# Optimization experiments

Measured on AMD Instinct MI355X. Metric: run time of the kernel, lower is better.

## Reference

```python
import jax, jax.numpy as jnp
import numpy as np


def _log_g(x):
    # log of g(x) = x + 0.5 for x >= 0, sigmoid(x) for x < 0 (minGRU paper, log-space)
    return jnp.where(x >= 0, jnp.log(jax.nn.relu(x) + 0.5), -jax.nn.softplus(-x))


def setup_inputs() -> dict:
    key = jax.random.key(0)
    k1, k2, k3 = jax.random.split(key, 3)
    B, L, D, H = 4, 8192, 512, 1024
    x = jax.random.normal(k1, (B, L, D), dtype=jnp.float32)
    # 1x1 conv in-projection to [hidden | gate], scaled for sane activation magnitudes
    W_in = jax.random.normal(k2, (2 * H, D), dtype=jnp.float32) * 0.05
    b_in = jnp.zeros((2 * H,), dtype=jnp.float32)
    # 1x1 conv out-projection back to model dim
    W_out = jax.random.normal(k3, (D, H), dtype=jnp.float32) * 0.05
    b_out = jnp.zeros((D,), dtype=jnp.float32)
    return {"x": x, "W_in": W_in, "b_in": b_in, "W_out": W_out, "b_out": b_out}


def reference(x, W_in, b_in, W_out, b_out):
    # x: [B, L, D]. tokenMixer transposes to [B, D, L] for MinGRU (1x1 convs),
    # which is equivalent to pointwise matmuls over the channel dim here.
    hg = jnp.einsum('bld,ed->ble', x, W_in) + b_in          # [B, L, 2H]
    H = hg.shape[-1] // 2
    hidden, gate = hg[..., :H], hg[..., H:]

    # minGRU log-space parallel scan (Heinsen associative scan):
    # h_t = (1 - z_t) * h_{t-1} + z_t * g(hidden_t), z_t = sigmoid(gate_t)
    log_coeffs = -jax.nn.softplus(gate)      # log(1 - z_t)
    log_z = -jax.nn.softplus(-gate)          # log(z_t)
    log_tilde_h = _log_g(hidden)             # log(g(hidden_t))

    a_star = jnp.cumsum(log_coeffs, axis=1)                              # [B, L, H]
    log_h = a_star + jax.lax.cumlogsumexp(log_z + log_tilde_h - a_star, axis=1)
    h = jnp.exp(log_h)                                                   # [B, L, H]

    out = jnp.einsum('blh,dh->bld', h, W_out) + b_out                    # [B, L, D]
    return out
```

## Files before the change

kernel.cpp:

```cpp
#include <hip/hip_runtime.h>
#include <hip/hip_bf16.h>
#include <cstdint>
#include <cstddef>

#define B_ 4
#define L_ 8192
#define D_ 512
#define H_ 1024
#define NC_ 256
#define LC_ (L_ / NC_)

typedef float  f32x4 __attribute__((ext_vector_type(4)));
typedef short  s16x8 __attribute__((ext_vector_type(8)));
typedef __bf16 b16x8 __attribute__((ext_vector_type(8)));

template <typename T, typename U>
__device__ inline auto mfma_sel(T a, T b, f32x4 c, U, int)
    -> decltype(__builtin_amdgcn_mfma_f32_16x16x32_bf16(a, b, c, 0, 0, 0)) {
  return __builtin_amdgcn_mfma_f32_16x16x32_bf16(a, b, c, 0, 0, 0);
}
template <typename T, typename U>
__device__ inline f32x4 mfma_sel(T a, T b, f32x4 c, U, long) {
  return __builtin_amdgcn_mfma_f32_16x16x32_bf16(
      __builtin_bit_cast(U, a), __builtin_bit_cast(U, b), c, 0, 0, 0);
}
__device__ inline f32x4 mfma_bf16_16x16x32(s16x8 a, s16x8 b, f32x4 c) {
  return mfma_sel(a, b, c, b16x8{}, 0);
}

__device__ inline ushort f2bf(float f) {
  uint32_t u = __builtin_bit_cast(uint32_t, f);
  uint32_t r = (u + 0x7fffu + ((u >> 16) & 1u)) >> 16;
  return (ushort)r;
}
__device__ inline float bf2f(ushort u) {
  return __builtin_bit_cast(float, (uint32_t)u << 16);
}

__global__ void cast_kernel(const float* __restrict__ in, ushort* __restrict__ out, int n4) {
  int i = blockIdx.x * blockDim.x + threadIdx.x;
  if (i >= n4) return;
  float4 f = reinterpret_cast<const float4*>(in)[i];
  ushort4 o;
  o.x = f2bf(f.x); o.y = f2bf(f.y); o.z = f2bf(f.z); o.w = f2bf(f.w);
  reinterpret_cast<ushort4*>(out)[i] = o;
}

__global__ void cast2_kernel(const float* __restrict__ in0, ushort* __restrict__ out0, int n4_0,
                             const float* __restrict__ in1, ushort* __restrict__ out1, int n4_1) {
  int i = blockIdx.x * blockDim.x + threadIdx.x;
  const float* in; ushort* out;
  if (i < n4_0) { in = in0; out = out0; }
  else { i -= n4_0; if (i >= n4_1) return; in = in1; out = out1; }
  float4 f = reinterpret_cast<const float4*>(in)[i];
  ushort4 o;
  o.x = f2bf(f.x); o.y = f2bf(f.y); o.z = f2bf(f.z); o.w = f2bf(f.w);
  reinterpret_cast<ushort4*>(out)[i] = o;
}

#define GLDS(srcp, dstp)                                                            \
  __builtin_amdgcn_global_load_lds(                                                 \
      (const __attribute__((address_space(1))) void*)(srcp),                        \
      (__attribute__((address_space(3))) void*)(dstp), 16, 0, 0)

#define BAR()                               \
  do {                                      \
    asm volatile("" ::: "memory");          \
    __builtin_amdgcn_s_barrier();           \
    asm volatile("" ::: "memory");          \
  } while (0)

template <bool OUT_BF16>
__global__ __launch_bounds__(512, 2)
void gemm_bt(const ushort* __restrict__ A, const ushort* __restrict__ Bm,
             const float* __restrict__ bias, void* __restrict__ Cv,
             int M, int N, int K) {
  __shared__ ushort As[2][256 * 64];
  __shared__ ushort Bs[2][256 * 64];
  const int tid  = threadIdx.x;
  const int wave = tid >> 6;
  const int lane = tid & 63;
  const int l15  = lane & 15;
  const int quad = lane >> 4;

  int id = blockIdx.y * gridDim.x + blockIdx.x;
  const int nwg = gridDim.x * gridDim.y;
  id = (id & 7) * (nwg >> 3) + (id >> 3);
  const int bxi = id % gridDim.x;
  const int byi = id / gridDim.x;

  const long bm = (long)byi * 256;
  const long bn = (long)bxi * 256;
  const int  wm = (wave >> 2) * 128;
  const int  wn = (wave & 3) * 64;

  f32x4 acc[8][4];
#pragma unroll
  for (int i = 0; i < 8; ++i)
#pragma unroll
    for (int j = 0; j < 4; ++j) acc[i][j] = (f32x4){0.f, 0.f, 0.f, 0.f};

  const int rl  = lane >> 3;
  const int cb  = (lane & 7) ^ rl;
  const int srow = wave * 32 + rl;
  const ushort* gA0 = A  + (bm + srow) * (long)K + cb * 8;
  const ushort* gB0 = Bm + (bn + srow) * (long)K + cb * 8;
  int ldst[4];
#pragma unroll
  for (int i = 0; i < 4; ++i) ldst[i] = (wave * 32 + 8 * i) * 64;

  const int sq0 = ((0 * 4 + quad) ^ (l15 & 7)) * 8;
  const int sq1 = ((1 * 4 + quad) ^ (l15 & 7)) * 8;
  int arow[8], brow[4];
#pragma unroll
  for (int i = 0; i < 8; ++i) arow[i] = (wm + i * 16 + l15) * 64;
#pragma unroll
  for (int j = 0; j < 4; ++j) brow[j] = (wn + j * 16 + l15) * 64;

  const int nkt = K >> 6;

#pragma unroll
  for (int i = 0; i < 4; ++i) GLDS(gA0 + 8L * i * K, &As[0][ldst[i]]);
#pragma unroll
  for (int i = 0; i < 4; ++i) GLDS(gB0 + 8L * i * K, &Bs[0][ldst[i]]);
  asm volatile("s_waitcnt vmcnt(0)" ::: "memory");
  BAR();

  for (int t = 0; t < nkt; ++t) {
    const int buf  = t & 1;
    const int nbuf = buf ^ 1;
    const bool pf  = (t + 1) < nkt;
    const ushort* Ac = As[buf];
    const ushort* Bc = Bs[buf];
    const long koff = (long)(t + 1) * 64;
    s16x8 bf[4], af[4];

#pragma unroll
    for (int j = 0; j < 4; ++j)
      bf[j] = *reinterpret_cast<const s16x8*>(&Bc[brow[j] + sq0]);
#pragma unroll
    for (int i = 0; i < 4; ++i)
      af[i] = *reinterpret_cast<const s16x8*>(&Ac[arow[i] + sq0]);
    if (pf) {
#pragma unroll
      for (int i = 0; i < 4; ++i) GLDS(gA0 + 8L * i * K + koff, &As[nbuf][ldst[i]]);
    }
    BAR();
    __builtin_amdgcn_s_setprio(1);
#pragma unroll
    for (int i = 0; i < 4; ++i)
#pragma unroll
      for (int j = 0; j < 4; ++j)
        acc[i][j] = mfma_bf16_16x16x32(af[i], bf[j], acc[i][j]);
    __builtin_amdgcn_s_setprio(0);
    BAR();

#pragma unroll
    for (int i = 0; i < 4; ++i)
      af[i] = *reinterpret_cast<const s16x8*>(&Ac[arow[4 + i] + sq0]);
    if (pf) {
#pragma unroll
      for (int i = 0; i < 4; ++i) GLDS(gB0 + 8L * i * K + koff, &Bs[nbuf][ldst[i]]);
    }
    BAR();
    __builtin_amdgcn_s_setprio(1);
#pragma unroll
    for (int i = 0; i < 4; ++i)
#pragma unroll
      for (int j = 0; j < 4; ++j)
        acc[4 + i][j] = mfma_bf16_16x16x32(af[i], bf[j], acc[4 + i][j]);
    __builtin_amdgcn_s_setprio(0);
    BAR();

#pragma unroll
    for (int j = 0; j < 4; ++j)
      bf[j] = *reinterpret_cast<const s16x8*>(&Bc[brow[j] + sq1]);
#pragma unroll
    for (int i = 0; i < 4; ++i)
      af[i] = *reinterpret_cast<const s16x8*>(&Ac[arow[i] + sq1]);
    BAR();
    __builtin_amdgcn_s_setprio(1);
#pragma unroll
    for (int i = 0; i < 4; ++i)
#pragma unroll
      for (int j = 0; j < 4; ++j)
        acc[i][j] = mfma_bf16_16x16x32(af[i], bf[j], acc[i][j]);
    __builtin_amdgcn_s_setprio(0);
    BAR();

#pragma unroll
    for (int i = 0; i < 4; ++i)
      af[i] = *reinterpret_cast<const s16x8*>(&Ac[arow[4 + i] + sq1]);
    BAR();
    __builtin_amdgcn_s_setprio(1);
#pragma unroll
    for (int i = 0; i < 4; ++i)
#pragma unroll
      for (int j = 0; j < 4; ++j)
        acc[4 + i][j] = mfma_bf16_16x16x32(af[i], bf[j], acc[4 + i][j]);
    __builtin_amdgcn_s_setprio(0);
    if (pf) asm volatile("s_waitcnt vmcnt(0)" ::: "memory");
    BAR();
  }

#pragma unroll
  for (int mi = 0; mi < 8; ++mi) {
    const long mrow = bm + wm + mi * 16 + quad * 4;
#pragma unroll
    for (int ni = 0; ni < 4; ++ni) {
      const long ncol = bn + wn + ni * 16 + l15;
      const float bv = bias[ncol];
      if (OUT_BF16) {
        ushort* cp = (ushort*)Cv + mrow * (long)N + ncol;
#pragma unroll
        for (int r = 0; r < 4; ++r) cp[(long)r * N] = f2bf(acc[mi][ni][r] + bv);
      } else {
        float* cp = (float*)Cv + mrow * (long)N + ncol;
#pragma unroll
        for (int r = 0; r < 4; ++r) cp[(long)r * N] = acc[mi][ni][r] + bv;
      }
    }
  }
}

__device__ inline float softplus_f(float x) {
  return fmaxf(x, 0.f) + __logf(1.f + __expf(-fabsf(x)));
}
__device__ inline float logaddexp_f(float a, float b) {
  float m = fmaxf(a, b);
  return m + __logf(1.f + __expf(-fabsf(a - b)));
}
__device__ inline void transform_f(float hd, float g, float& lc, float& v) {
  float sp = softplus_f(g);
  lc = -sp;
  float lz = g - sp;
  float lth = (hd >= 0.f) ? __logf(hd + 0.5f) : (hd - softplus_f(hd));
  v = lz + lth;
}

__global__ void scan_phase1(const ushort* __restrict__ hg,
                            float* __restrict__ Ac, float* __restrict__ Bc) {
  int gid = blockIdx.x * blockDim.x + threadIdx.x;
  int hq = gid & (H_ / 4 - 1);
  int c  = (gid >> 8) & (NC_ - 1);
  int b  = gid >> 16;
  const ushort* p = hg + ((size_t)(b * L_ + c * LC_) * (2 * H_)) + hq * 4;
  float As[4] = {0.f, 0.f, 0.f, 0.f};
  float Bv[4] = {-INFINITY, -INFINITY, -INFINITY, -INFINITY};
#pragma unroll 4
  for (int l = 0; l < LC_; ++l) {
    ushort4 hd4 = *reinterpret_cast<const ushort4*>(p);
    ushort4 g4  = *reinterpret_cast<const ushort4*>(p + H_);
    float hdv[4] = {bf2f(hd4.x), bf2f(hd4.y), bf2f(hd4.z), bf2f(hd4.w)};
    float gv[4]  = {bf2f(g4.x),  bf2f(g4.y),  bf2f(g4.z),  bf2f(g4.w)};
#pragma unroll
    for (int j = 0; j < 4; ++j) {
      float lc, v; transform_f(hdv[j], gv[j], lc, v);
      As[j] += lc;
      Bv[j] = logaddexp_f(Bv[j] + lc, v);
    }
    p += 2 * H_;
  }
  size_t o = (size_t)(b * NC_ + c) * H_ + hq * 4;
  *reinterpret_cast<float4*>(&Ac[o]) = make_float4(As[0], As[1], As[2], As[3]);
  *reinterpret_cast<float4*>(&Bc[o]) = make_float4(Bv[0], Bv[1], Bv[2], Bv[3]);
}

__global__ void scan_phase2(const float* __restrict__ Ac, const float* __restrict__ Bc,
                            float* __restrict__ carry) {
  int gid = blockIdx.x * blockDim.x + threadIdx.x;
  int h = gid & (H_ - 1);
  int b = gid >> 10;
  float P = -INFINITY;
  for (int c = 0; c < NC_; ++c) {
    size_t o = (size_t)(b * NC_ + c) * H_ + h;
    carry[o] = P;
    P = logaddexp_f(P + Ac[o], Bc[o]);
  }
}

__global__ void scan_phase3(const ushort* __restrict__ hg, const float* __restrict__ carry,
                            ushort* __restrict__ hb) {
  int gid = blockIdx.x * blockDim.x + threadIdx.x;
  int hq = gid & (H_ / 4 - 1);
  int c  = (gid >> 8) & (NC_ - 1);
  int b  = gid >> 16;
  float4 cr = *reinterpret_cast<const float4*>(&carry[(size_t)(b * NC_ + c) * H_ + hq * 4]);
  float lh[4] = {cr.x, cr.y, cr.z, cr.w};
  const ushort* p = hg + ((size_t)(b * L_ + c * LC_) * (2 * H_)) + hq * 4;
  ushort* q = hb + (size_t)(b * L_ + c * LC_) * H_ + hq * 4;
#pragma unroll 4
  for (int l = 0; l < LC_; ++l) {
    ushort4 hd4 = *reinterpret_cast<const ushort4*>(p);
    ushort4 g4  = *reinterpret_cast<const ushort4*>(p + H_);
    float hdv[4] = {bf2f(hd4.x), bf2f(hd4.y), bf2f(hd4.z), bf2f(hd4.w)};
    float gv[4]  = {bf2f(g4.x),  bf2f(g4.y),  bf2f(g4.z),  bf2f(g4.w)};
    ushort4 o;
    ushort* op = &o.x;
#pragma unroll
    for (int j = 0; j < 4; ++j) {
      float lc, v; transform_f(hdv[j], gv[j], lc, v);
      lh[j] = logaddexp_f(lh[j] + lc, v);
      op[j] = f2bf(__expf(lh[j]));
    }
    *reinterpret_cast<ushort4*>(q) = o;
    p += 2 * H_;
    q += H_;
  }
}

extern "C" void kernel_launch(void* const* d_in, const int* in_sizes, int n_in,
                              void* d_out, int out_size, void* d_ws, size_t ws_size,
                              hipStream_t stream) {
  const float* x     = (const float*)d_in[0];
  const float* W_in  = (const float*)d_in[1];
  const float* b_in  = (const float*)d_in[2];
  const float* W_out = (const float*)d_in[3];
  const float* b_out = (const float*)d_in[4];
  float* out = (float*)d_out;

  char* ws = (char*)d_ws;
  size_t off = 0;
  auto alloc = [&](size_t bytes) {
    void* p = ws + off;
    off = (off + bytes + 255) & ~(size_t)255;
    return p;
  };
  ushort* xb    = (ushort*)alloc((size_t)B_ * L_ * H_ * 2);
  ushort* hb    = xb;
  ushort* Wib   = (ushort*)alloc((size_t)2 * H_ * D_ * 2);
  ushort* Wob   = (ushort*)alloc((size_t)D_ * H_ * 2);
  ushort* hgb   = (ushort*)alloc((size_t)B_ * L_ * 2 * H_ * 2);
  float*  Ac    = (float*)alloc((size_t)B_ * NC_ * H_ * 4);
  float*  Bc    = (float*)alloc((size_t)B_ * NC_ * H_ * 4);
  float*  carry = (float*)alloc((size_t)B_ * NC_ * H_ * 4);

  cast_kernel<<<(B_ * L_ * D_ / 4 + 255) / 256, 256, 0, stream>>>(x, xb, B_ * L_ * D_ / 4);
  {
    int n0 = 2 * H_ * D_ / 4, n1 = D_ * H_ / 4;
    cast2_kernel<<<(n0 + n1 + 255) / 256, 256, 0, stream>>>(W_in, Wib, n0, W_out, Wob, n1);
  }

  gemm_bt<true><<<dim3((2 * H_) / 256, (B_ * L_) / 256), 512, 0, stream>>>(
      xb, Wib, b_in, hgb, B_ * L_, 2 * H_, D_);

  scan_phase1<<<(B_ * NC_ * H_ / 4) / 256, 256, 0, stream>>>(hgb, Ac, Bc);
  scan_phase2<<<(B_ * H_) / 256, 256, 0, stream>>>(Ac, Bc, carry);
  scan_phase3<<<(B_ * NC_ * H_ / 4) / 256, 256, 0, stream>>>(hgb, carry, hb);

  gemm_bt<false><<<dim3(D_ / 256, (B_ * L_) / 256), 512, 0, stream>>>(
      hb, Wob, b_out, out, B_ * L_, D_, H_);
}
```

Baseline: 423.7 us.

## Fuse log-space gate transform into in-projection GEMM epilogue

```diff
diff --git a/kernel.cpp b/kernel.cpp
--- a/kernel.cpp
+++ b/kernel.cpp
@@ -35,6 +35,21 @@
 }
 __device__ inline float bf2f(ushort u) {
   return __builtin_bit_cast(float, (uint32_t)u << 16);
+}
+
+__device__ inline float softplus_f(float x) {
+  return fmaxf(x, 0.f) + __logf(1.f + __expf(-fabsf(x)));
+}
+__device__ inline float logaddexp_f(float a, float b) {
+  float m = fmaxf(a, b);
+  return m + __logf(1.f + __expf(-fabsf(a - b)));
+}
+__device__ inline void transform_f(float hd, float g, float& lc, float& v) {
+  float sp = softplus_f(g);
+  lc = -sp;
+  float lz = g - sp;
+  float lth = (hd >= 0.f) ? __logf(hd + 0.5f) : (hd - softplus_f(hd));
+  v = lz + lth;
 }
 
 __global__ void cast_kernel(const float* __restrict__ in, ushort* __restrict__ out, int n4) {
@@ -70,7 +85,7 @@
     asm volatile("" ::: "memory");          \
   } while (0)
 
-template <bool OUT_BF16>
+template <int MODE>
 __global__ __launch_bounds__(512, 2)
 void gemm_bt(const ushort* __restrict__ A, const ushort* __restrict__ Bm,
              const float* __restrict__ bias, void* __restrict__ Cv,
@@ -92,7 +107,6 @@
   const long bm = (long)byi * 256;
   const long bn = (long)bxi * 256;
   const int  wm = (wave >> 2) * 128;
-  const int  wn = (wave & 3) * 64;
 
   f32x4 acc[8][4];
 #pragma unroll
@@ -103,8 +117,15 @@
   const int rl  = lane >> 3;
   const int cb  = (lane & 7) ^ rl;
   const int srow = wave * 32 + rl;
-  const ushort* gA0 = A  + (bm + srow) * (long)K + cb * 8;
-  const ushort* gB0 = Bm + (bn + srow) * (long)K + cb * 8;
+  const ushort* gA0 = A + (bm + srow) * (long)K + cb * 8;
+  const ushort* gB0;
+  if (MODE == 1) {
+    const long n0 = bn >> 1;
+    const long grow = (srow < 128) ? (n0 + srow) : (1024 + n0 + (srow - 128));
+    gB0 = Bm + grow * (long)K + cb * 8;
+  } else {
+    gB0 = Bm + (bn + srow) * (long)K + cb * 8;
+  }
   int ldst[4];
 #pragma unroll
   for (int i = 0; i < 4; ++i) ldst[i] = (wave * 32 + 8 * i) * 64;
@@ -114,8 +135,18 @@
   int arow[8], brow[4];
 #pragma unroll
   for (int i = 0; i < 8; ++i) arow[i] = (wm + i * 16 + l15) * 64;
-#pragma unroll
-  for (int j = 0; j < 4; ++j) brow[j] = (wn + j * 16 + l15) * 64;
+  if (MODE == 1) {
+    const int wn0 = (wave & 3) * 32;
+#pragma unroll
+    for (int j = 0; j < 4; ++j) {
+      const int trow = (j < 2) ? (wn0 + j * 16) : (128 + wn0 + (j - 2) * 16);
+      brow[j] = (trow + l15) * 64;
+    }
+  } else {
+    const int wn = (wave & 3) * 64;
+#pragma unroll
+    for (int j = 0; j < 4; ++j) brow[j] = (wn + j * 16 + l15) * 64;
+  }
 
   const int nkt = K >> 6;
 
@@ -203,39 +234,43 @@
     BAR();
   }
 
-#pragma unroll
-  for (int mi = 0; mi < 8; ++mi) {
-    const long mrow = bm + wm + mi * 16 + quad * 4;
-#pragma unroll
-    for (int ni = 0; ni < 4; ++ni) {
-      const long ncol = bn + wn + ni * 16 + l15;
-      const float bv = bias[ncol];
-      if (OUT_BF16) {
-        ushort* cp = (ushort*)Cv + mrow * (long)N + ncol;
-#pragma unroll
-        for (int r = 0; r < 4; ++r) cp[(long)r * N] = f2bf(acc[mi][ni][r] + bv);
-      } else {
+  if (MODE == 1) {
+    const long n0  = bn >> 1;
+    const int  wn0 = (wave & 3) * 32;
+#pragma unroll
+    for (int mi = 0; mi < 8; ++mi) {
+      const long mrow = bm + wm + mi * 16 + quad * 4;
+#pragma unroll
+      for (int j = 0; j < 2; ++j) {
+        const long ch = n0 + wn0 + j * 16 + l15;
+        const float bh = bias[ch];
+        const float bg = bias[(long)(N >> 1) + ch];
+        ushort* lp = (ushort*)Cv + mrow * (long)N + ch;
+#pragma unroll
+        for (int r = 0; r < 4; ++r) {
+          float hd = acc[mi][j][r] + bh;
+          float g  = acc[mi][j + 2][r] + bg;
+          float lc, v; transform_f(hd, g, lc, v);
+          lp[(long)r * N] = f2bf(lc);
+          lp[(long)r * N + (N >> 1)] = f2bf(v);
+        }
+      }
+    }
+  } else {
+    const int wn = (wave & 3) * 64;
+#pragma unroll
+    for (int mi = 0; mi < 8; ++mi) {
+      const long mrow = bm + wm + mi * 16 + quad * 4;
+#pragma unroll
+      for (int ni = 0; ni < 4; ++ni) {
+        const long ncol = bn + wn + ni * 16 + l15;
+        const float bv = bias[ncol];
         float* cp = (float*)Cv + mrow * (long)N + ncol;
 #pragma unroll
         for (int r = 0; r < 4; ++r) cp[(long)r * N] = acc[mi][ni][r] + bv;
       }
     }
   }
-}
-
-__device__ inline float softplus_f(float x) {
-  return fmaxf(x, 0.f) + __logf(1.f + __expf(-fabsf(x)));
-}
-__device__ inline float logaddexp_f(float a, float b) {
-  float m = fmaxf(a, b);
-  return m + __logf(1.f + __expf(-fabsf(a - b)));
-}
-__device__ inline void transform_f(float hd, float g, float& lc, float& v) {
-  float sp = softplus_f(g);
-  lc = -sp;
-  float lz = g - sp;
-  float lth = (hd >= 0.f) ? __logf(hd + 0.5f) : (hd - softplus_f(hd));
-  v = lz + lth;
 }
 
 __global__ void scan_phase1(const ushort* __restrict__ hg,
@@ -249,15 +284,14 @@
   float Bv[4] = {-INFINITY, -INFINITY, -INFINITY, -INFINITY};
 #pragma unroll 4
   for (int l = 0; l < LC_; ++l) {
-    ushort4 hd4 = *reinterpret_cast<const ushort4*>(p);
-    ushort4 g4  = *reinterpret_cast<const ushort4*>(p + H_);
-    float hdv[4] = {bf2f(hd4.x), bf2f(hd4.y), bf2f(hd4.z), bf2f(hd4.w)};
-    float gv[4]  = {bf2f(g4.x),  bf2f(g4.y),  bf2f(g4.z),  bf2f(g4.w)};
+    ushort4 lc4 = *reinterpret_cast<const ushort4*>(p);
+    ushort4 v4  = *reinterpret_cast<const ushort4*>(p + H_);
+    float lcv[4] = {bf2f(lc4.x), bf2f(lc4.y), bf2f(lc4.z), bf2f(lc4.w)};
+    float vv[4]  = {bf2f(v4.x),  bf2f(v4.y),  bf2f(v4.z),  bf2f(v4.w)};
 #pragma unroll
     for (int j = 0; j < 4; ++j) {
-      float lc, v; transform_f(hdv[j], gv[j], lc, v);
-      As[j] += lc;
-      Bv[j] = logaddexp_f(Bv[j] + lc, v);
+      As[j] += lcv[j];
+      Bv[j] = logaddexp_f(Bv[j] + lcv[j], vv[j]);
     }
     p += 2 * H_;
   }
@@ -291,16 +325,15 @@
   ushort* q = hb + (size_t)(b * L_ + c * LC_) * H_ + hq * 4;
 #pragma unroll 4
   for (int l = 0; l < LC_; ++l) {
-    ushort4 hd4 = *reinterpret_cast<const ushort4*>(p);
-    ushort4 g4  = *reinterpret_cast<const ushort4*>(p + H_);
-    float hdv[4] = {bf2f(hd4.x), bf2f(hd4.y), bf2f(hd4.z), bf2f(hd4.w)};
-    float gv[4]  = {bf2f(g4.x),  bf2f(g4.y),  bf2f(g4.z),  bf2f(g4.w)};
+    ushort4 lc4 = *reinterpret_cast<const ushort4*>(p);
+    ushort4 v4  = *reinterpret_cast<const ushort4*>(p + H_);
+    float lcv[4] = {bf2f(lc4.x), bf2f(lc4.y), bf2f(lc4.z), bf2f(lc4.w)};
+    float vv[4]  = {bf2f(v4.x),  bf2f(v4.y),  bf2f(v4.z),  bf2f(v4.w)};
     ushort4 o;
     ushort* op = &o.x;
 #pragma unroll
     for (int j = 0; j < 4; ++j) {
-      float lc, v; transform_f(hdv[j], gv[j], lc, v);
-      lh[j] = logaddexp_f(lh[j] + lc, v);
+      lh[j] = logaddexp_f(lh[j] + lcv[j], vv[j]);
       op[j] = f2bf(__expf(lh[j]));
     }
     *reinterpret_cast<ushort4*>(q) = o;
@@ -341,13 +374,13 @@
     cast2_kernel<<<(n0 + n1 + 255) / 256, 256, 0, stream>>>(W_in, Wib, n0, W_out, Wob, n1);
   }
 
-  gemm_bt<true><<<dim3((2 * H_) / 256, (B_ * L_) / 256), 512, 0, stream>>>(
+  gemm_bt<1><<<dim3((2 * H_) / 256, (B_ * L_) / 256), 512, 0, stream>>>(
       xb, Wib, b_in, hgb, B_ * L_, 2 * H_, D_);
 
   scan_phase1<<<(B_ * NC_ * H_ / 4) / 256, 256, 0, stream>>>(hgb, Ac, Bc);
   scan_phase2<<<(B_ * H_) / 256, 256, 0, stream>>>(Ac, Bc, carry);
   scan_phase3<<<(B_ * NC_ * H_ / 4) / 256, 256, 0, stream>>>(hgb, carry, hb);
 
-  gemm_bt<false><<<dim3(D_ / 256, (B_ * L_) / 256), 512, 0, stream>>>(
+  gemm_bt<0><<<dim3(D_ / 256, (B_ * L_) / 256), 512, 0, stream>>>(
       hb, Wob, b_out, out, B_ * L_, D_, H_);
 }
```

Result: faster. 386.4 us (-8.8%).
